# Kernel optimization log

Measured on AMD Instinct MI355X. Metric: run time of the kernel, lower is better.

The kernel has to match this reference:

```python
import math
import jax, jax.numpy as jnp
import numpy as np

D_MODEL = 768
N_HEADS = 12


def setup_inputs() -> dict:
    key = jax.random.key(0)
    kx, kw, kb = jax.random.split(key, 3)
    x = jax.random.normal(kx, (2, 2048, D_MODEL), dtype=jnp.float32)
    # nn.Linear(D, 3D): weight [3D, D], bias [3D]; init ~ U(-1/sqrt(D), 1/sqrt(D))
    bound = 1.0 / math.sqrt(D_MODEL)
    W_kqv = jax.random.uniform(kw, (3 * D_MODEL, D_MODEL), dtype=jnp.float32, minval=-bound, maxval=bound)
    b_kqv = jax.random.uniform(kb, (3 * D_MODEL,), dtype=jnp.float32, minval=-bound, maxval=bound)
    return {"x": x, "W_kqv": W_kqv, "b_kqv": b_kqv}


def reference(x, W_kqv, b_kqv):
    N, C, D = x.shape
    H = N_HEADS
    hd = D // H
    z = jnp.einsum('ncd,ed->nce', x, W_kqv) + b_kqv  # [N, C, 3D]
    # order in source: k first, then q, then v
    k = z[:, :, :D].reshape(N, C, H, hd).transpose(0, 2, 1, 3)       # [N,H,C,hd]
    q = z[:, :, D:2 * D].reshape(N, C, H, hd).transpose(0, 2, 1, 3)
    v = z[:, :, 2 * D:].reshape(N, C, H, hd).transpose(0, 2, 1, 3)
    # NOTE: faithful to source: scale by sqrt(D) (full model dim), not sqrt(head_dim)
    scores = jnp.einsum('nhqd,nhkd->nhqk', q, k) / math.sqrt(D)
    causal = jnp.tril(jnp.ones((C, C), dtype=bool))
    scores = jnp.where(causal, scores, -jnp.inf)
    attn = jax.nn.softmax(scores, axis=-1)
    out = jnp.einsum('nhqk,nhkd->nhqd', attn, v)  # [N,H,C,hd]
    return out.transpose(0, 2, 1, 3).reshape(N, C, D)
```

## Files before the change

### kernel.cpp

```cpp
#include <hip/hip_runtime.h>
#include <stdint.h>

#define D_MODEL 768
#define E3      2304
#define NCTX    2048
#define NH      12
#define HD      64
#define MROWS   4096
#define NHTOT   24

typedef __attribute__((ext_vector_type(8))) short short8;
typedef __attribute__((ext_vector_type(4))) short bf16x4;
typedef __attribute__((ext_vector_type(4))) float f32x4;

typedef __attribute__((address_space(3))) uint32_t lds_u32;
typedef __attribute__((address_space(1))) uint32_t glob_u32;

__device__ __forceinline__ void async_copy16(const void* g, void* l) {
    __builtin_amdgcn_global_load_lds((const glob_u32*)(uintptr_t)g,
                                     (lds_u32*)(uint32_t)(uintptr_t)l, 16, 0, 0);
}

__device__ __forceinline__ unsigned short f2bf(float f) {
    uint32_t u = __builtin_bit_cast(uint32_t, f);
    u += 0x7fffu + ((u >> 16) & 1u);
    return (unsigned short)(u >> 16);
}

__device__ __forceinline__ float fast_exp2(float x) {
#if __has_builtin(__builtin_amdgcn_exp2f)
    return __builtin_amdgcn_exp2f(x);
#else
    return __expf(x * 0.6931471805599453f);
#endif
}

#if __has_builtin(__builtin_amdgcn_mfma_f32_16x16x16bf16_1k)
#define HAVE_MFMA16 1
#else
#define HAVE_MFMA16 0
#endif

__global__ void cast_bf16_kernel(const float* __restrict__ in, unsigned short* __restrict__ out) {
    int i = blockIdx.x * blockDim.x + threadIdx.x;
    float4 v = ((const float4*)in)[i];
    ushort4 o;
    o.x = f2bf(v.x); o.y = f2bf(v.y); o.z = f2bf(v.z); o.w = f2bf(v.w);
    ((ushort4*)out)[i] = o;
}

__global__ __launch_bounds__(256) void qkv_gemm(const unsigned short* __restrict__ A,
                                                const unsigned short* __restrict__ B,
                                                const float* __restrict__ bias,
                                                unsigned short* __restrict__ Zq,
                                                unsigned short* __restrict__ Kb,
                                                unsigned short* __restrict__ Vb) {
    __shared__ __attribute__((aligned(16))) unsigned short sA[128 * 64];
    __shared__ __attribute__((aligned(16))) unsigned short sB[128 * 64];

    const int tid  = threadIdx.x;
    const int wave = tid >> 6;
    const int lane = tid & 63;
    const int quad = lane >> 4;
    const int l15  = lane & 15;
    const int wm   = (wave >> 1) << 6;
    const int wn   = (wave & 1) << 6;
    const int row0 = blockIdx.y * 128;
    const int col0 = blockIdx.x * 128;

    const int srow   = lane >> 3;
    const int schunk = (lane & 7) * 8;

    f32x4 acc[4][4] = {};

    for (int k0 = 0; k0 < D_MODEL; k0 += 64) {
        __syncthreads();
#pragma unroll
        for (int c = 0; c < 4; ++c) {
            const int rbase = wave * 32 + c * 8;
            async_copy16(A + (size_t)(row0 + rbase + srow) * D_MODEL + k0 + schunk, &sA[rbase * 64]);
            async_copy16(B + (size_t)(col0 + rbase + srow) * D_MODEL + k0 + schunk, &sB[rbase * 64]);
        }
        __syncthreads();

#pragma unroll
        for (int ks = 0; ks < 2; ++ks) {
            short8 aF[4], bF[4];
#pragma unroll
            for (int i = 0; i < 4; ++i)
                aF[i] = *(const short8*)&sA[(wm + i * 16 + l15) * 64 + ks * 32 + quad * 8];
#pragma unroll
            for (int i = 0; i < 4; ++i)
                bF[i] = *(const short8*)&sB[(wn + i * 16 + l15) * 64 + ks * 32 + quad * 8];
#pragma unroll
            for (int i = 0; i < 4; ++i)
#pragma unroll
                for (int j = 0; j < 4; ++j)
                    acc[i][j] = __builtin_amdgcn_mfma_f32_16x16x32_bf16(aF[i], bF[j], acc[i][j], 0, 0, 0);
        }
    }

    if (col0 < D_MODEL) {
#pragma unroll
        for (int j = 0; j < 4; ++j) {
            const int col = col0 + wn + j * 16 + l15;
            const float bv = bias[col];
            const int h = col >> 6, d = col & 63;
            const int ks = d >> 5, quadd = (d >> 3) & 3, e = d & 7;
#pragma unroll
            for (int i = 0; i < 4; ++i) {
                const int row = row0 + wm + i * 16 + quad * 4;
                const int n = row >> 11;
                const int key = row & (NCTX - 1);
                const int kb = key >> 6;
                const int ct = i;
                const size_t base = ((size_t)((n * NH + h) * 32 + kb)) * 4096
                                  + (((ks * 4 + ct) * 4 + quadd) * 16) * 8 + e;
#pragma unroll
                for (int r = 0; r < 4; ++r)
                    Kb[base + (size_t)(quad * 4 + r) * 8] = f2bf(acc[i][j][r] + bv);
            }
        }
    } else if (col0 < 2 * D_MODEL) {
        const float zscale = 0.036084391824351615f * 1.4426950408889634f;
#pragma unroll
        for (int j = 0; j < 4; ++j) {
            const int col = col0 - D_MODEL + wn + j * 16 + l15;
            const float bv = bias[col0 + wn + j * 16 + l15];
#pragma unroll
            for (int i = 0; i < 4; ++i) {
                const int row = row0 + wm + i * 16 + quad * 4;
#pragma unroll
                for (int r = 0; r < 4; ++r)
                    Zq[(size_t)(row + r) * D_MODEL + col] = f2bf((acc[i][j][r] + bv) * zscale);
            }
        }
    } else {
#pragma unroll
        for (int j = 0; j < 4; ++j) {
            const int col = col0 + wn + j * 16 + l15;
            const float bv = bias[col];
            const int ch = col - 2 * D_MODEL;
            const int h = ch >> 6, d = ch & 63;
            const int dt = d >> 4, l15d = d & 15;
#pragma unroll
            for (int i = 0; i < 4; ++i) {
                const int row = row0 + wm + i * 16 + quad * 4;
                const int n = row >> 11;
                const int key = row & (NCTX - 1);
                const int kb = key >> 6;
                const int ct = i, quadv = quad;
                ushort4 w4;
                w4.x = f2bf(acc[i][j][0] + bv);
                w4.y = f2bf(acc[i][j][1] + bv);
                w4.z = f2bf(acc[i][j][2] + bv);
                w4.w = f2bf(acc[i][j][3] + bv);
                *(ushort4*)&Vb[((size_t)((n * NH + h) * 32 + kb)) * 4096
                               + (((ct * 4 + dt) * 4 + quadv) * 16 + l15d) * 4] = w4;
            }
        }
    }
}

__global__ __launch_bounds__(256) void attn_kernel(const unsigned short* __restrict__ Zq,
                                                   const unsigned short* __restrict__ Kb,
                                                   const unsigned short* __restrict__ Vb,
                                                   float* __restrict__ out) {
    __shared__ __attribute__((aligned(16))) unsigned short sK[2][4096];
    __shared__ __attribute__((aligned(16))) unsigned short sV[2][4096];
#if !HAVE_MFMA16
    __shared__ __attribute__((aligned(16))) unsigned short sP[4][16 * 72];
#endif

    const int tid  = threadIdx.x;
    const int wave = tid >> 6;
    const int lane = tid & 63;
    const int quad = lane >> 4;
    const int l15  = lane & 15;
    const int b    = blockIdx.x;
    const int t    = (NCTX / 64 - 1) - b / NHTOT;
    const int nh   = b - (b / NHTOT) * NHTOT;
    const int n    = nh / NH;
    const int h    = nh - n * NH;

    const unsigned short* KbP = Kb + (size_t)(nh * 32) * 4096;
    const unsigned short* VbP = Vb + (size_t)(nh * 32) * 4096;

    const unsigned short* Qp = Zq + (size_t)(n * NCTX + t * 64 + wave * 16) * D_MODEL + h * HD;
    short8 qf[2];
#pragma unroll
    for (int ks = 0; ks < 2; ++ks)
        qf[ks] = *(const short8*)&Qp[(size_t)l15 * D_MODEL + ks * 32 + quad * 8];

    f32x4 o[4] = {};
    float lsum = 0.0f;

#pragma unroll
    for (int c = 0; c < 2; ++c) {
        const int off = wave * 1024 + c * 512;
        async_copy16(KbP + off + lane * 8, &sK[0][off]);
        async_copy16(VbP + off + lane * 8, &sV[0][off]);
    }

    for (int kb = 0; kb <= t; ++kb) {
        const int buf = kb & 1;
        __syncthreads();
        if (kb < t) {
#pragma unroll
            for (int c = 0; c < 2; ++c) {
                const int off = wave * 1024 + c * 512;
                async_copy16(KbP + (size_t)(kb + 1) * 4096 + off + lane * 8, &sK[buf ^ 1][off]);
                async_copy16(VbP + (size_t)(kb + 1) * 4096 + off + lane * 8, &sV[buf ^ 1][off]);
            }
        }

        short8 kf[2][4];
#pragma unroll
        for (int ks = 0; ks < 2; ++ks)
#pragma unroll
            for (int ct = 0; ct < 4; ++ct)
                kf[ks][ct] = *(const short8*)&sK[buf][(ks * 4 + ct) * 512 + lane * 8];

        f32x4 s[4] = {};
#pragma unroll
        for (int ct = 0; ct < 4; ++ct) {
            s[ct] = __builtin_amdgcn_mfma_f32_16x16x32_bf16(kf[0][ct], qf[0], s[ct], 0, 0, 0);
            s[ct] = __builtin_amdgcn_mfma_f32_16x16x32_bf16(kf[1][ct], qf[1], s[ct], 0, 0, 0);
        }

        const bool diag = (kb == t);
        const int qg = t * 64 + wave * 16 + l15;
#if HAVE_MFMA16
        bf16x4 pA[4];
#endif
#pragma unroll
        for (int ct = 0; ct < 4; ++ct) {
            float pv[4];
#pragma unroll
            for (int r = 0; r < 4; ++r) {
                const int key = kb * 64 + ct * 16 + quad * 4 + r;
                float sv = s[ct][r];
                if (diag && key > qg) sv = -INFINITY;
                pv[r] = fast_exp2(sv);
                lsum += pv[r];
            }
#if HAVE_MFMA16
            pA[ct][0] = (short)f2bf(pv[0]); pA[ct][1] = (short)f2bf(pv[1]);
            pA[ct][2] = (short)f2bf(pv[2]); pA[ct][3] = (short)f2bf(pv[3]);
#else
            ushort4 w4;
            w4.x = f2bf(pv[0]); w4.y = f2bf(pv[1]); w4.z = f2bf(pv[2]); w4.w = f2bf(pv[3]);
            *(ushort4*)&sP[wave][l15 * 72 + ct * 16 + quad * 4] = w4;
#endif
        }

#if HAVE_MFMA16
#pragma unroll
        for (int ct = 0; ct < 4; ++ct)
#pragma unroll
            for (int dt = 0; dt < 4; ++dt) {
                const bf16x4 vf = *(const bf16x4*)&sV[buf][(ct * 4 + dt) * 256 + lane * 4];
                o[dt] = __builtin_amdgcn_mfma_f32_16x16x16bf16_1k(pA[ct], vf, o[dt], 0, 0, 0);
            }
#else
        const short8 pf0 = *(const short8*)&sP[wave][l15 * 72 + quad * 8];
        const short8 pf1 = *(const short8*)&sP[wave][l15 * 72 + 32 + quad * 8];
#pragma unroll
        for (int dt = 0; dt < 4; ++dt) {
            short8 vf0, vf1;
#pragma unroll
            for (int e = 0; e < 8; ++e) {
                const int k0 = quad * 8 + e;
                const int k1 = 32 + quad * 8 + e;
                vf0[e] = (short)sV[buf][(((k0 >> 4) * 4 + dt) * 4 + ((k0 >> 2) & 3)) * 64 + l15 * 4 + (k0 & 3)];
                vf1[e] = (short)sV[buf][(((k1 >> 4) * 4 + dt) * 4 + ((k1 >> 2) & 3)) * 64 + l15 * 4 + (k1 & 3)];
            }
            o[dt] = __builtin_amdgcn_mfma_f32_16x16x32_bf16(pf0, vf0, o[dt], 0, 0, 0);
            o[dt] = __builtin_amdgcn_mfma_f32_16x16x32_bf16(pf1, vf1, o[dt], 0, 0, 0);
        }
#endif
    }

    float l = lsum;
    l += __shfl_xor(l, 16);
    l += __shfl_xor(l, 32);
    const float linv = 1.0f / l;
#pragma unroll
    for (int r = 0; r < 4; ++r) {
        const float inv = __shfl(linv, quad * 4 + r);
        const size_t row = (size_t)n * NCTX + t * 64 + wave * 16 + quad * 4 + r;
#pragma unroll
        for (int dt = 0; dt < 4; ++dt)
            out[row * D_MODEL + h * HD + dt * 16 + l15] = o[dt][r] * inv;
    }
}

extern "C" void kernel_launch(void* const* d_in, const int* in_sizes, int n_in,
                              void* d_out, int out_size, void* d_ws, size_t ws_size,
                              hipStream_t stream) {
    const float* x = (const float*)d_in[0];
    const float* W = (const float*)d_in[1];
    const float* b = (const float*)d_in[2];
    float* out = (float*)d_out;

    unsigned short* xb = (unsigned short*)d_ws;
    unsigned short* Wb = xb + (size_t)MROWS * D_MODEL;
    unsigned short* Zq = Wb + (size_t)E3 * D_MODEL;
    unsigned short* Kb = Zq + (size_t)MROWS * D_MODEL;
    unsigned short* Vb = Kb + (size_t)NHTOT * 32 * 4096;

    cast_bf16_kernel<<<dim3((MROWS * D_MODEL / 4) / 256), 256, 0, stream>>>(x, xb);
    cast_bf16_kernel<<<dim3((E3 * D_MODEL / 4) / 256), 256, 0, stream>>>(W, Wb);
    qkv_gemm<<<dim3(E3 / 128, MROWS / 128), 256, 0, stream>>>(xb, Wb, b, Zq, Kb, Vb);
    attn_kernel<<<dim3(NHTOT * (NCTX / 64)), 256, 0, stream>>>(Zq, Kb, Vb, out);
}
```

Measured before the change: 146.7 us.

## Use two waves per attention block, each handling 32 query rows, and fuse casts

Attention blocks now launch with 128 threads instead of 256. Each wave processes two 16-row query groups, so each K/V fragment read from LDS is reused across both groups, and s_setprio is raised around the MFMA sections. The two fp32-to-bf16 cast launches are merged into one kernel that switches source on the index. This reduces LDS traffic per FLOP and launch overhead, at the cost of higher register pressure and fewer waves per block to hide latency.

```diff
diff --git a/kernel.cpp b/kernel.cpp
--- a/kernel.cpp
+++ b/kernel.cpp
@@ -41,12 +41,21 @@
 #define HAVE_MFMA16 0
 #endif
 
-__global__ void cast_bf16_kernel(const float* __restrict__ in, unsigned short* __restrict__ out) {
+__global__ __launch_bounds__(256) void cast2_bf16_kernel(const float* __restrict__ a,
+                                                         unsigned short* __restrict__ oa,
+                                                         int na4,
+                                                         const float* __restrict__ b,
+                                                         unsigned short* __restrict__ ob) {
     int i = blockIdx.x * blockDim.x + threadIdx.x;
-    float4 v = ((const float4*)in)[i];
+    const float4* src;
+    ushort4* dst;
+    int idx;
+    if (i < na4) { src = (const float4*)a; dst = (ushort4*)oa; idx = i; }
+    else         { src = (const float4*)b; dst = (ushort4*)ob; idx = i - na4; }
+    float4 v = src[idx];
     ushort4 o;
     o.x = f2bf(v.x); o.y = f2bf(v.y); o.z = f2bf(v.z); o.w = f2bf(v.w);
-    ((ushort4*)out)[i] = o;
+    dst[idx] = o;
 }
 
 __global__ __launch_bounds__(256) void qkv_gemm(const unsigned short* __restrict__ A,
@@ -162,14 +171,14 @@
     }
 }
 
-__global__ __launch_bounds__(256) void attn_kernel(const unsigned short* __restrict__ Zq,
+__global__ __launch_bounds__(128) void attn_kernel(const unsigned short* __restrict__ Zq,
                                                    const unsigned short* __restrict__ Kb,
                                                    const unsigned short* __restrict__ Vb,
                                                    float* __restrict__ out) {
     __shared__ __attribute__((aligned(16))) unsigned short sK[2][4096];
     __shared__ __attribute__((aligned(16))) unsigned short sV[2][4096];
 #if !HAVE_MFMA16
-    __shared__ __attribute__((aligned(16))) unsigned short sP[4][16 * 72];
+    __shared__ __attribute__((aligned(16))) unsigned short sP[2][16 * 72];
 #endif
 
     const int tid  = threadIdx.x;
@@ -186,18 +195,20 @@
     const unsigned short* KbP = Kb + (size_t)(nh * 32) * 4096;
     const unsigned short* VbP = Vb + (size_t)(nh * 32) * 4096;
 
-    const unsigned short* Qp = Zq + (size_t)(n * NCTX + t * 64 + wave * 16) * D_MODEL + h * HD;
-    short8 qf[2];
-#pragma unroll
-    for (int ks = 0; ks < 2; ++ks)
-        qf[ks] = *(const short8*)&Qp[(size_t)l15 * D_MODEL + ks * 32 + quad * 8];
-
-    f32x4 o[4] = {};
-    float lsum = 0.0f;
-
-#pragma unroll
-    for (int c = 0; c < 2; ++c) {
-        const int off = wave * 1024 + c * 512;
+    const unsigned short* Qp = Zq + (size_t)(n * NCTX + t * 64 + wave * 32) * D_MODEL + h * HD;
+    short8 qf[2][2];
+#pragma unroll
+    for (int g = 0; g < 2; ++g)
+#pragma unroll
+        for (int ks = 0; ks < 2; ++ks)
+            qf[g][ks] = *(const short8*)&Qp[(size_t)(g * 16 + l15) * D_MODEL + ks * 32 + quad * 8];
+
+    f32x4 o[2][4] = {};
+    float lsum[2] = {0.0f, 0.0f};
+
+#pragma unroll
+    for (int c = 0; c < 4; ++c) {
+        const int off = wave * 2048 + c * 512;
         async_copy16(KbP + off + lane * 8, &sK[0][off]);
         async_copy16(VbP + off + lane * 8, &sV[0][off]);
     }
@@ -207,8 +218,8 @@
         __syncthreads();
         if (kb < t) {
 #pragma unroll
-            for (int c = 0; c < 2; ++c) {
-                const int off = wave * 1024 + c * 512;
+            for (int c = 0; c < 4; ++c) {
+                const int off = wave * 2048 + c * 512;
                 async_copy16(KbP + (size_t)(kb + 1) * 4096 + off + lane * 8, &sK[buf ^ 1][off]);
                 async_copy16(VbP + (size_t)(kb + 1) * 4096 + off + lane * 8, &sV[buf ^ 1][off]);
             }
@@ -221,77 +232,90 @@
             for (int ct = 0; ct < 4; ++ct)
                 kf[ks][ct] = *(const short8*)&sK[buf][(ks * 4 + ct) * 512 + lane * 8];
 
-        f32x4 s[4] = {};
-#pragma unroll
-        for (int ct = 0; ct < 4; ++ct) {
-            s[ct] = __builtin_amdgcn_mfma_f32_16x16x32_bf16(kf[0][ct], qf[0], s[ct], 0, 0, 0);
-            s[ct] = __builtin_amdgcn_mfma_f32_16x16x32_bf16(kf[1][ct], qf[1], s[ct], 0, 0, 0);
-        }
-
         const bool diag = (kb == t);
-        const int qg = t * 64 + wave * 16 + l15;
 #if HAVE_MFMA16
-        bf16x4 pA[4];
-#endif
-#pragma unroll
-        for (int ct = 0; ct < 4; ++ct) {
-            float pv[4];
-#pragma unroll
-            for (int r = 0; r < 4; ++r) {
-                const int key = kb * 64 + ct * 16 + quad * 4 + r;
-                float sv = s[ct][r];
-                if (diag && key > qg) sv = -INFINITY;
-                pv[r] = fast_exp2(sv);
-                lsum += pv[r];
-            }
+        bf16x4 pA[2][4];
+#endif
+#pragma unroll
+        for (int g = 0; g < 2; ++g) {
+            f32x4 s[4] = {};
+            __builtin_amdgcn_s_setprio(1);
+#pragma unroll
+            for (int ct = 0; ct < 4; ++ct) {
+                s[ct] = __builtin_amdgcn_mfma_f32_16x16x32_bf16(kf[0][ct], qf[g][0], s[ct], 0, 0, 0);
+                s[ct] = __builtin_amdgcn_mfma_f32_16x16x32_bf16(kf[1][ct], qf[g][1], s[ct], 0, 0, 0);
+            }
+            __builtin_amdgcn_s_setprio(0);
+
+            const int qg = t * 64 + wave * 32 + g * 16 + l15;
+#pragma unroll
+            for (int ct = 0; ct < 4; ++ct) {
+                float pv[4];
+#pragma unroll
+                for (int r = 0; r < 4; ++r) {
+                    const int key = kb * 64 + ct * 16 + quad * 4 + r;
+                    float sv = s[ct][r];
+                    if (diag && key > qg) sv = -INFINITY;
+                    pv[r] = fast_exp2(sv);
+                    lsum[g] += pv[r];
+                }
 #if HAVE_MFMA16
-            pA[ct][0] = (short)f2bf(pv[0]); pA[ct][1] = (short)f2bf(pv[1]);
-            pA[ct][2] = (short)f2bf(pv[2]); pA[ct][3] = (short)f2bf(pv[3]);
+                pA[g][ct][0] = (short)f2bf(pv[0]); pA[g][ct][1] = (short)f2bf(pv[1]);
+                pA[g][ct][2] = (short)f2bf(pv[2]); pA[g][ct][3] = (short)f2bf(pv[3]);
 #else
-            ushort4 w4;
-            w4.x = f2bf(pv[0]); w4.y = f2bf(pv[1]); w4.z = f2bf(pv[2]); w4.w = f2bf(pv[3]);
-            *(ushort4*)&sP[wave][l15 * 72 + ct * 16 + quad * 4] = w4;
+                ushort4 w4;
+                w4.x = f2bf(pv[0]); w4.y = f2bf(pv[1]); w4.z = f2bf(pv[2]); w4.w = f2bf(pv[3]);
+                *(ushort4*)&sP[wave][l15 * 72 + ct * 16 + quad * 4] = w4;
+#endif
+            }
+
+#if !HAVE_MFMA16
+            const short8 pf0 = *(const short8*)&sP[wave][l15 * 72 + quad * 8];
+            const short8 pf1 = *(const short8*)&sP[wave][l15 * 72 + 32 + quad * 8];
+#pragma unroll
+            for (int dt = 0; dt < 4; ++dt) {
+                short8 vf0, vf1;
+#pragma unroll
+                for (int e = 0; e < 8; ++e) {
+                    const int k0 = quad * 8 + e;
+                    const int k1 = 32 + quad * 8 + e;
+                    vf0[e] = (short)sV[buf][(((k0 >> 4) * 4 + dt) * 4 + ((k0 >> 2) & 3)) * 64 + l15 * 4 + (k0 & 3)];
+                    vf1[e] = (short)sV[buf][(((k1 >> 4) * 4 + dt) * 4 + ((k1 >> 2) & 3)) * 64 + l15 * 4 + (k1 & 3)];
+                }
+                o[g][dt] = __builtin_amdgcn_mfma_f32_16x16x32_bf16(pf0, vf0, o[g][dt], 0, 0, 0);
+                o[g][dt] = __builtin_amdgcn_mfma_f32_16x16x32_bf16(pf1, vf1, o[g][dt], 0, 0, 0);
+            }
 #endif
         }
 
 #if HAVE_MFMA16
+        __builtin_amdgcn_s_setprio(1);
 #pragma unroll
         for (int ct = 0; ct < 4; ++ct)
 #pragma unroll
             for (int dt = 0; dt < 4; ++dt) {
                 const bf16x4 vf = *(const bf16x4*)&sV[buf][(ct * 4 + dt) * 256 + lane * 4];
-                o[dt] = __builtin_amdgcn_mfma_f32_16x16x16bf16_1k(pA[ct], vf, o[dt], 0, 0, 0);
-            }
-#else
-        const short8 pf0 = *(const short8*)&sP[wave][l15 * 72 + quad * 8];
-        const short8 pf1 = *(const short8*)&sP[wave][l15 * 72 + 32 + quad * 8];
-#pragma unroll
-        for (int dt = 0; dt < 4; ++dt) {
-            short8 vf0, vf1;
-#pragma unroll
-            for (int e = 0; e < 8; ++e) {
-                const int k0 = quad * 8 + e;
-                const int k1 = 32 + quad * 8 + e;
-                vf0[e] = (short)sV[buf][(((k0 >> 4) * 4 + dt) * 4 + ((k0 >> 2) & 3)) * 64 + l15 * 4 + (k0 & 3)];
-                vf1[e] = (short)sV[buf][(((k1 >> 4) * 4 + dt) * 4 + ((k1 >> 2) & 3)) * 64 + l15 * 4 + (k1 & 3)];
-            }
-            o[dt] = __builtin_amdgcn_mfma_f32_16x16x32_bf16(pf0, vf0, o[dt], 0, 0, 0);
-            o[dt] = __builtin_amdgcn_mfma_f32_16x16x32_bf16(pf1, vf1, o[dt], 0, 0, 0);
-        }
-#endif
-    }
-
-    float l = lsum;
-    l += __shfl_xor(l, 16);
-    l += __shfl_xor(l, 32);
-    const float linv = 1.0f / l;
-#pragma unroll
-    for (int r = 0; r < 4; ++r) {
-        const float inv = __shfl(linv, quad * 4 + r);
-        const size_t row = (size_t)n * NCTX + t * 64 + wave * 16 + quad * 4 + r;
-#pragma unroll
-        for (int dt = 0; dt < 4; ++dt)
-            out[row * D_MODEL + h * HD + dt * 16 + l15] = o[dt][r] * inv;
+                o[0][dt] = __builtin_amdgcn_mfma_f32_16x16x16bf16_1k(pA[0][ct], vf, o[0][dt], 0, 0, 0);
+                o[1][dt] = __builtin_amdgcn_mfma_f32_16x16x16bf16_1k(pA[1][ct], vf, o[1][dt], 0, 0, 0);
+            }
+        __builtin_amdgcn_s_setprio(0);
+#endif
+    }
+
+#pragma unroll
+    for (int g = 0; g < 2; ++g) {
+        float l = lsum[g];
+        l += __shfl_xor(l, 16);
+        l += __shfl_xor(l, 32);
+        const float linv = 1.0f / l;
+#pragma unroll
+        for (int r = 0; r < 4; ++r) {
+            const float inv = __shfl(linv, quad * 4 + r);
+            const size_t row = (size_t)n * NCTX + t * 64 + wave * 32 + g * 16 + quad * 4 + r;
+#pragma unroll
+            for (int dt = 0; dt < 4; ++dt)
+                out[row * D_MODEL + h * HD + dt * 16 + l15] = o[g][dt][r] * inv;
+        }
     }
 }
 
@@ -309,8 +333,9 @@
     unsigned short* Kb = Zq + (size_t)MROWS * D_MODEL;
     unsigned short* Vb = Kb + (size_t)NHTOT * 32 * 4096;
 
-    cast_bf16_kernel<<<dim3((MROWS * D_MODEL / 4) / 256), 256, 0, stream>>>(x, xb);
-    cast_bf16_kernel<<<dim3((E3 * D_MODEL / 4) / 256), 256, 0, stream>>>(W, Wb);
+    const int NA4 = MROWS * D_MODEL / 4;
+    const int NW4 = E3 * D_MODEL / 4;
+    cast2_bf16_kernel<<<dim3((NA4 + NW4) / 256), 256, 0, stream>>>(x, xb, NA4, W, Wb);
     qkv_gemm<<<dim3(E3 / 128, MROWS / 128), 256, 0, stream>>>(xb, Wb, b, Zq, Kb, Vb);
-    attn_kernel<<<dim3(NHTOT * (NCTX / 64)), 256, 0, stream>>>(Zq, Kb, Vb, out);
-}
+    attn_kernel<<<dim3(NHTOT * (NCTX / 64)), 128, 0, stream>>>(Zq, Kb, Vb, out);
+}
```

Measured after the change: 164.7 us. +12.3%, slower.
